# Kernel tuning notes

Measured on AMD Instinct MI355X. Metric: run time of the kernel, lower is better.

Reference implementation:

```python
import jax, jax.numpy as jnp
import numpy as np

M, IN, OUT, R = 8192, 4096, 4096, 16  # tokens, in_features, out_features, lora rank


def setup_inputs() -> dict:
    key = jax.random.key(0)
    k = jax.random.split(key, 7)
    # symmetric int8 quantized activations and weights
    x = jax.random.randint(k[0], (M, IN), -127, 128, dtype=jnp.int8)
    weight = jax.random.randint(k[1], (OUT, IN), -127, 128, dtype=jnp.int8)
    # per-token activation scales and per-output-channel weight scales
    x_scales = jax.random.uniform(k[2], (M,), jnp.float32, 0.5, 1.5) / 127.0
    scales = jax.random.uniform(k[3], (OUT,), jnp.float32, 0.5, 1.5) / 127.0
    bias = jax.random.normal(k[4], (OUT,), jnp.float32)
    # module inits lora_a ~ N(0, 1/r); lora_b is zeros in the module but we use
    # small random values so the LoRA path is numerically exercised
    lora_a = jax.random.normal(k[5], (R, IN), jnp.float32) * (1.0 / R)
    lora_b = jax.random.normal(k[6], (OUT, R), jnp.float32) * 0.02
    return dict(x=x, weight=weight, bias=bias, x_scales=x_scales,
                scales=scales, lora_a=lora_a, lora_b=lora_b, fuse_gelu=1)


def reference(x, weight, bias, x_scales, scales, lora_a, lora_b, fuse_gelu):
    acc = jax.lax.dot_general(x, weight, (((1,), (1,)), ((), ())),
                              preferred_element_type=jnp.int32)
    # dequantize with outer product of per-token and per-channel scales
    main = acc.astype(jnp.float32) * x_scales[:, None] * scales[None, :]
    # LoRA correction on the dequantized activations: (x_deq @ A^T) @ B^T
    x_deq = x.astype(jnp.float32) * x_scales[:, None]          # [M, IN]
    lora = (x_deq @ lora_a.T) @ lora_b.T                        # [M, R] @ [R, OUT]
    out = main + lora + bias[None, :]
    if fuse_gelu:  # static Python flag
        out = jax.nn.gelu(out, approximate=True)  # tanh-approx GELU (CUDA fused path)
    return out
```

## Files before the change

kernel.cpp:

```cpp
#include <hip/hip_runtime.h>

#define M_DIM 8192
#define IN_DIM 4096
#define OUT_DIM 4096

typedef int   v4i __attribute__((ext_vector_type(4)));
typedef short v8s __attribute__((ext_vector_type(8)));
typedef float v4f __attribute__((ext_vector_type(4)));

static __device__ __forceinline__ int pack4(int a, int b, int c, int d) {
    return (a & 255) | ((b & 255) << 8) | ((c & 255) << 16) | ((d & 255) << 24);
}

static __device__ __forceinline__ short f2bf(float f) {
    unsigned u = __float_as_uint(f);
    u = (u + 0x7FFFu + ((u >> 16) & 1u)) >> 16;
    return (short)u;
}

static __device__ __forceinline__ short i2bf(int v) {
    float f = (float)v;
    return (short)(__float_as_uint(f) >> 16);
}

static __device__ __forceinline__ float gelu_tanh(float u) {
    float u2 = u * u;
    float p  = fmaf(u2, 0.0356774081f, 0.7978845608f);
    float v  = u * p;
    float e  = __builtin_amdgcn_exp2f(v * 2.8853900818f);
    return u - u * __builtin_amdgcn_rcpf(e + 1.0f);
}

static __device__ __forceinline__ void async_cp16(const signed char* g, signed char* l) {
    __builtin_amdgcn_global_load_lds((const __attribute__((address_space(1))) void*)g,
                                     (__attribute__((address_space(3))) void*)l, 16, 0, 0);
}

__global__ __launch_bounds__(256) void pack_i32_i8_kernel(const int* __restrict__ src,
                                                          signed char* __restrict__ dst) {
    const int t = threadIdx.x;
    const size_t blk = (size_t)blockIdx.x;
    const int4* p = (const int4*)src + blk * 1024;
    int* q = (int*)dst + blk * 1024;
    int4 v0 = p[t], v1 = p[256 + t], v2 = p[512 + t], v3 = p[768 + t];
    q[t]       = pack4(v0.x, v0.y, v0.z, v0.w);
    q[256 + t] = pack4(v1.x, v1.y, v1.z, v1.w);
    q[512 + t] = pack4(v2.x, v2.y, v2.z, v2.w);
    q[768 + t] = pack4(v3.x, v3.y, v3.z, v3.w);
}

__global__ __launch_bounds__(256) void pack_a_kernel(const float* __restrict__ la,
                                                     short* __restrict__ a16) {
    size_t i = ((size_t)blockIdx.x * 256 + threadIdx.x) * 8;
    const float4* p = (const float4*)(la + i);
    float4 a = p[0], b = p[1];
    v8s o;
    o[0] = f2bf(a.x); o[1] = f2bf(a.y); o[2] = f2bf(a.z); o[3] = f2bf(a.w);
    o[4] = f2bf(b.x); o[5] = f2bf(b.y); o[6] = f2bf(b.z); o[7] = f2bf(b.w);
    *(v8s*)(a16 + i) = o;
}

__global__ __launch_bounds__(256) void lora_t_kernel(const signed char* __restrict__ x8,
                                                     const short* __restrict__ a16,
                                                     float* __restrict__ T) {
    __shared__ float red[4 * 256];
    const int tid = threadIdx.x;
    const int lane = tid & 63, wv = tid >> 6;
    const int fr = lane & 15, fq = lane >> 4;
    const int m0 = blockIdx.x * 16;

    const signed char* bx = x8 + (size_t)(m0 + fr) * IN_DIM + wv * 1024 + fq * 8;
    const short*       ba = a16 + (size_t)fr * IN_DIM + wv * 1024 + fq * 8;

    v4f acc = {0.f, 0.f, 0.f, 0.f};
#pragma unroll 4
    for (int kt = 0; kt < 32; ++kt) {
        int2 w = *(const int2*)(bx + kt * 32);
        int lo = w.x, hi = w.y;
        v8s xa;
        xa[0] = i2bf((lo << 24) >> 24); xa[1] = i2bf((lo << 16) >> 24);
        xa[2] = i2bf((lo << 8) >> 24);  xa[3] = i2bf(lo >> 24);
        xa[4] = i2bf((hi << 24) >> 24); xa[5] = i2bf((hi << 16) >> 24);
        xa[6] = i2bf((hi << 8) >> 24);  xa[7] = i2bf(hi >> 24);
        v8s aa = *(const v8s*)(ba + kt * 32);
        acc = __builtin_amdgcn_mfma_f32_16x16x32_bf16(xa, aa, acc, 0, 0, 0);
    }
    *(v4f*)&red[wv * 256 + lane * 4] = acc;
    __syncthreads();

    float s = red[tid] + red[256 + tid] + red[512 + tid] + red[768 + tid];
    int sl = tid >> 2, j = tid & 3;
    int row = ((sl >> 4) << 2) + j, col = sl & 15;
    T[(size_t)(m0 + row) * 16 + col] = s;
}

__global__ __launch_bounds__(256, 4) void q8_gemm_kernel(
    const signed char* __restrict__ x8, const signed char* __restrict__ w8,
    const float* __restrict__ T, const float* __restrict__ lb,
    const float* __restrict__ bias, const float* __restrict__ xsc,
    const float* __restrict__ wsc, const int* __restrict__ gflag,
    float* __restrict__ out) {
    __shared__ __align__(16) signed char smem[32768];

    const int tid  = threadIdx.x;
    const int lane = tid & 63;
    const int wv   = tid >> 6;
    const int wm   = wv >> 1;
    const int wn   = wv & 1;
    const int bn   = blockIdx.x & 31;
    const int bm   = blockIdx.x >> 5;
    const int fr   = lane & 15;
    const int fq   = lane >> 4;

    const int srow = wv * 32 + (lane >> 2);
    const int scol = (((lane & 3) ^ ((lane >> 2) & 3)) & 3) * 16;
    const signed char* ag0 = x8 + (size_t)(bm * 128 + srow) * IN_DIM + scol;
    const signed char* ag1 = ag0 + 16 * IN_DIM;
    const signed char* bg0 = w8 + (size_t)(bn * 128 + srow) * IN_DIM + scol;
    const signed char* bg1 = bg0 + 16 * IN_DIM;
    signed char* sA0 = smem + wv * 2048;
    signed char* sB0 = smem + 8192 + wv * 2048;
    signed char* sA1 = smem + 16384 + wv * 2048;
    signed char* sB1 = smem + 24576 + wv * 2048;

    v4i acc[4][4];
#pragma unroll
    for (int i = 0; i < 4; ++i)
#pragma unroll
        for (int j = 0; j < 4; ++j) acc[i][j] = 0;

    const int rot    = ((fq ^ fr) & 3) * 16;
    const int abase0 = (wm * 64 + fr) * 64 + rot;
    const int bbase0 = (wn * 64 + fr) * 64 + rot;

    async_cp16(ag0, sA0); async_cp16(ag1, sA0 + 1024);
    async_cp16(bg0, sB0); async_cp16(bg1, sB0 + 1024);

#pragma unroll 2
    for (int kk = 0; kk < 64; ++kk) {
        __syncthreads();
        if (kk + 1 < 64) {
            const size_t ko = (size_t)(kk + 1) * 64;
            if (kk & 1) {
                async_cp16(ag0 + ko, sA0); async_cp16(ag1 + ko, sA0 + 1024);
                async_cp16(bg0 + ko, sB0); async_cp16(bg1 + ko, sB0 + 1024);
            } else {
                async_cp16(ag0 + ko, sA1); async_cp16(ag1 + ko, sA1 + 1024);
                async_cp16(bg0 + ko, sB1); async_cp16(bg1 + ko, sB1 + 1024);
            }
        }
        const signed char* Ab = smem + ((kk & 1) ? 16384 : 0);
        const signed char* Bb = Ab + 8192;

        v4i av[4], bv[4];
#pragma unroll
        for (int mt = 0; mt < 4; ++mt) av[mt] = *(const v4i*)(Ab + abase0 + mt * 1024);
#pragma unroll
        for (int nt = 0; nt < 4; ++nt) bv[nt] = *(const v4i*)(Bb + bbase0 + nt * 1024);
#pragma unroll
        for (int mt = 0; mt < 4; ++mt)
#pragma unroll
            for (int nt = 0; nt < 4; ++nt)
                acc[mt][nt] = __builtin_amdgcn_mfma_i32_16x16x64_i8(av[mt], bv[nt],
                                                                    acc[mt][nt], 0, 0, 0);
    }

    __syncthreads();
    short* Tb     = (short*)smem;
    short* Bbs    = (short*)(smem + 8192);
    float* xs_t   = (float*)(smem + 16384);
    float* ws_t   = xs_t + 128;
    float* bias_t = ws_t + 128;

    {
        const int row = tid >> 1, half = tid & 1;
        const float4* tp = (const float4*)(T + (size_t)(bm * 128 + row) * 16 + half * 8);
        float4 f0 = tp[0], f1 = tp[1];
        short* dst = &Tb[row * 32 + half * 8];
        dst[0] = f2bf(f0.x); dst[1] = f2bf(f0.y); dst[2] = f2bf(f0.z); dst[3] = f2bf(f0.w);
        dst[4] = f2bf(f1.x); dst[5] = f2bf(f1.y); dst[6] = f2bf(f1.z); dst[7] = f2bf(f1.w);
        short* dz = &Tb[row * 32 + 16 + half * 8];
#pragma unroll
        for (int j = 0; j < 8; ++j) dz[j] = 0;

        const float4* bp = (const float4*)(lb + (size_t)(bn * 128 + row) * 16 + half * 8);
        float4 g0 = bp[0], g1 = bp[1];
        short* db = &Bbs[row * 32 + half * 8];
        db[0] = f2bf(g0.x); db[1] = f2bf(g0.y); db[2] = f2bf(g0.z); db[3] = f2bf(g0.w);
        db[4] = f2bf(g1.x); db[5] = f2bf(g1.y); db[6] = f2bf(g1.z); db[7] = f2bf(g1.w);
        short* dbz = &Bbs[row * 32 + 16 + half * 8];
#pragma unroll
        for (int j = 0; j < 8; ++j) dbz[j] = 0;
    }
    if (tid < 128) {
        xs_t[tid]   = xsc[bm * 128 + tid];
        ws_t[tid]   = wsc[bn * 128 + tid];
        bias_t[tid] = bias[bn * 128 + tid];
    }
    __syncthreads();

    const bool dg = (*gflag) != 0;

    v8s tb[4], bbf[4];
#pragma unroll
    for (int mt = 0; mt < 4; ++mt)
        tb[mt] = *(const v8s*)(&Tb[(wm * 64 + mt * 16 + fr) * 32 + fq * 8]);
#pragma unroll
    for (int nt = 0; nt < 4; ++nt)
        bbf[nt] = *(const v8s*)(&Bbs[(wn * 64 + nt * 16 + fr) * 32 + fq * 8]);

#pragma unroll
    for (int mt = 0; mt < 4; ++mt) {
#pragma unroll
        for (int nt = 0; nt < 4; ++nt) {
            const int ncol  = wn * 64 + nt * 16 + fr;
            const float wsv = ws_t[ncol];
            const float bv  = bias_t[ncol];
            v4f fa;
            fa[0] = (float)acc[mt][nt][0] * wsv;
            fa[1] = (float)acc[mt][nt][1] * wsv;
            fa[2] = (float)acc[mt][nt][2] * wsv;
            fa[3] = (float)acc[mt][nt][3] * wsv;
            fa = __builtin_amdgcn_mfma_f32_16x16x32_bf16(tb[mt], bbf[nt], fa, 0, 0, 0);
#pragma unroll
            for (int r = 0; r < 4; ++r) {
                const int ml = wm * 64 + mt * 16 + fq * 4 + r;
                float u = fmaf(xs_t[ml], fa[r], bv);
                if (dg) u = gelu_tanh(u);
                out[(size_t)(bm * 128 + ml) * OUT_DIM + bn * 128 + ncol] = u;
            }
        }
    }
}

extern "C" void kernel_launch(void* const* d_in, const int* in_sizes, int n_in,
                              void* d_out, int out_size, void* d_ws, size_t ws_size,
                              hipStream_t stream) {
    const int*   x     = (const int*)d_in[0];
    const int*   wt    = (const int*)d_in[1];
    const float* bias  = (const float*)d_in[2];
    const float* xsc   = (const float*)d_in[3];
    const float* wsc   = (const float*)d_in[4];
    const float* la    = (const float*)d_in[5];
    const float* lb    = (const float*)d_in[6];
    const int*   gflag = (const int*)d_in[7];
    float* out = (float*)d_out;

    signed char* x8 = (signed char*)d_ws;
    signed char* w8 = x8 + (size_t)M_DIM * IN_DIM;
    float* T = (float*)(w8 + (size_t)OUT_DIM * IN_DIM);
    short* a16 = (short*)w8;

    pack_i32_i8_kernel<<<(size_t)M_DIM * IN_DIM / 4096, 256, 0, stream>>>(x, x8);
    pack_a_kernel<<<16 * IN_DIM / (8 * 256), 256, 0, stream>>>(la, a16);
    lora_t_kernel<<<M_DIM / 16, 256, 0, stream>>>(x8, a16, T);
    pack_i32_i8_kernel<<<(size_t)OUT_DIM * IN_DIM / 4096, 256, 0, stream>>>(wt, w8);
    q8_gemm_kernel<<<(M_DIM / 128) * (OUT_DIM / 128), 256, 0, stream>>>(
        x8, w8, T, lb, bias, xsc, wsc, gflag, out);
}
```

Measured before the change: 454.5 us.

## Use 256x256 tiles with 32x32 MFMA, pre-tiled operands, fused x pack

The int8 GEMM moves from 128x128 to 256x256 block tiles using 32x32x32 i8 MFMAs. Operands are packed into an MFMA-fragment-ordered layout so each lane's LDS reads are contiguous. Packing x is fused into the LoRA T kernel, and blocks are remapped across XCDs for L2 locality. The aim is more operand reuse per byte loaded and fewer launches and passes over memory. The cost is 64KB of LDS, one block per CU, and a larger register footprint.

```diff
diff --git a/kernel.cpp b/kernel.cpp
--- a/kernel.cpp
+++ b/kernel.cpp
@@ -4,9 +4,11 @@
 #define IN_DIM 4096
 #define OUT_DIM 4096
 
-typedef int   v4i __attribute__((ext_vector_type(4)));
-typedef short v8s __attribute__((ext_vector_type(8)));
-typedef float v4f __attribute__((ext_vector_type(4)));
+typedef int   v4i  __attribute__((ext_vector_type(4)));
+typedef int   v16i __attribute__((ext_vector_type(16)));
+typedef short v8s  __attribute__((ext_vector_type(8)));
+typedef float v4f  __attribute__((ext_vector_type(4)));
+typedef float v16f __attribute__((ext_vector_type(16)));
 
 static __device__ __forceinline__ int pack4(int a, int b, int c, int d) {
     return (a & 255) | ((b & 255) << 8) | ((c & 255) << 16) | ((d & 255) << 24);
@@ -36,18 +38,6 @@
                                      (__attribute__((address_space(3))) void*)l, 16, 0, 0);
 }
 
-__global__ __launch_bounds__(256) void pack_i32_i8_kernel(const int* __restrict__ src,
-                                                          signed char* __restrict__ dst) {
-    const int t = threadIdx.x;
-    const size_t blk = (size_t)blockIdx.x;
-    const int4* p = (const int4*)src + blk * 1024;
-    int* q = (int*)dst + blk * 1024;
-    int4 v0 = p[t], v1 = p[256 + t], v2 = p[512 + t], v3 = p[768 + t];
-    q[t]       = pack4(v0.x, v0.y, v0.z, v0.w);
-    q[256 + t] = pack4(v1.x, v1.y, v1.z, v1.w);
-    q[512 + t] = pack4(v2.x, v2.y, v2.z, v2.w);
-    q[768 + t] = pack4(v3.x, v3.y, v3.z, v3.w);
-}
 
 __global__ __launch_bounds__(256) void pack_a_kernel(const float* __restrict__ la,
                                                      short* __restrict__ a16) {
@@ -60,174 +50,191 @@
     *(v8s*)(a16 + i) = o;
 }
 
-__global__ __launch_bounds__(256) void lora_t_kernel(const signed char* __restrict__ x8,
-                                                     const short* __restrict__ a16,
-                                                     float* __restrict__ T) {
+__global__ __launch_bounds__(256) void pack_w_kernel(const int* __restrict__ w,
+                                                     signed char* __restrict__ w8t) {
+    const int flat = blockIdx.x * 256 + threadIdx.x;
+    const int l  = flat & 63;
+    const int gp = (flat >> 6) & 15;
+    const int kk = (flat >> 10) & 63;
+    const int bn = flat >> 16;
+    const int n = bn * 256 + ((gp >> 1) << 5) + (l & 31);
+    const int k = kk * 64 + ((gp & 1) << 5) + ((l >> 5) << 4);
+    const int4* p = (const int4*)(w + (size_t)n * IN_DIM + k);
+    int4 a = p[0], b = p[1], c = p[2], d = p[3];
+    int4 o;
+    o.x = pack4(a.x, a.y, a.z, a.w);
+    o.y = pack4(b.x, b.y, b.z, b.w);
+    o.z = pack4(c.x, c.y, c.z, c.w);
+    o.w = pack4(d.x, d.y, d.z, d.w);
+    *(int4*)(w8t + (size_t)flat * 16) = o;
+}
+
+__global__ __launch_bounds__(256) void pack_x_lora_kernel(const int* __restrict__ x,
+                                                          const short* __restrict__ a16,
+                                                          signed char* __restrict__ x8t,
+                                                          float* __restrict__ T) {
     __shared__ float red[4 * 256];
     const int tid = threadIdx.x;
     const int lane = tid & 63, wv = tid >> 6;
     const int fr = lane & 15, fq = lane >> 4;
     const int m0 = blockIdx.x * 16;
-
-    const signed char* bx = x8 + (size_t)(m0 + fr) * IN_DIM + wv * 1024 + fq * 8;
-    const short*       ba = a16 + (size_t)fr * IN_DIM + wv * 1024 + fq * 8;
+    const int bm = m0 >> 8;
+    const int g  = (m0 >> 5) & 7;
+    const int l5 = (m0 & 16) + fr;
+    const int row = m0 + fr;
 
     v4f acc = {0.f, 0.f, 0.f, 0.f};
-#pragma unroll 4
+#pragma unroll 2
     for (int kt = 0; kt < 32; ++kt) {
-        int2 w = *(const int2*)(bx + kt * 32);
-        int lo = w.x, hi = w.y;
+        const int k  = wv * 1024 + kt * 32 + fq * 8;
+        const int4* xp = (const int4*)(x + (size_t)row * IN_DIM + k);
+        int4 a = xp[0], b = xp[1];
+        const int kk = k >> 6, c = (k >> 4) & 3, j8 = (k >> 3) & 1;
+        int2 pk = make_int2(pack4(a.x, a.y, a.z, a.w), pack4(b.x, b.y, b.z, b.w));
+        *(int2*)(x8t + ((size_t)((bm * 64 + kk) * 16 + g * 2 + (c >> 1))) * 1024 +
+                 ((c & 1) * 32 + l5) * 16 + j8 * 8) = pk;
         v8s xa;
-        xa[0] = i2bf((lo << 24) >> 24); xa[1] = i2bf((lo << 16) >> 24);
-        xa[2] = i2bf((lo << 8) >> 24);  xa[3] = i2bf(lo >> 24);
-        xa[4] = i2bf((hi << 24) >> 24); xa[5] = i2bf((hi << 16) >> 24);
-        xa[6] = i2bf((hi << 8) >> 24);  xa[7] = i2bf(hi >> 24);
-        v8s aa = *(const v8s*)(ba + kt * 32);
+        xa[0] = i2bf(a.x); xa[1] = i2bf(a.y); xa[2] = i2bf(a.z); xa[3] = i2bf(a.w);
+        xa[4] = i2bf(b.x); xa[5] = i2bf(b.y); xa[6] = i2bf(b.z); xa[7] = i2bf(b.w);
+        v8s aa = *(const v8s*)(a16 + (size_t)fr * IN_DIM + k);
         acc = __builtin_amdgcn_mfma_f32_16x16x32_bf16(xa, aa, acc, 0, 0, 0);
     }
     *(v4f*)&red[wv * 256 + lane * 4] = acc;
     __syncthreads();
 
     float s = red[tid] + red[256 + tid] + red[512 + tid] + red[768 + tid];
-    int sl = tid >> 2, j = tid & 3;
-    int row = ((sl >> 4) << 2) + j, col = sl & 15;
-    T[(size_t)(m0 + row) * 16 + col] = s;
-}
-
-__global__ __launch_bounds__(256, 4) void q8_gemm_kernel(
-    const signed char* __restrict__ x8, const signed char* __restrict__ w8,
-    const float* __restrict__ T, const float* __restrict__ lb,
+    const int sl = tid >> 2, j = tid & 3;
+    const int r16 = ((sl >> 4) << 2) + j, col = sl & 15;
+    T[(size_t)(m0 + r16) * 16 + col] = s;
+}
+
+__global__ __launch_bounds__(256, 1) void q8_gemm_kernel(
+    const signed char* __restrict__ x8t, const signed char* __restrict__ w8t,
+    const float* __restrict__ Tp, const float* __restrict__ lbm,
     const float* __restrict__ bias, const float* __restrict__ xsc,
     const float* __restrict__ wsc, const int* __restrict__ gflag,
     float* __restrict__ out) {
-    __shared__ __align__(16) signed char smem[32768];
+    __shared__ __align__(16) signed char smem[65536];
 
     const int tid  = threadIdx.x;
     const int lane = tid & 63;
     const int wv   = tid >> 6;
-    const int wm   = wv >> 1;
-    const int wn   = wv & 1;
-    const int bn   = blockIdx.x & 31;
-    const int bm   = blockIdx.x >> 5;
-    const int fr   = lane & 15;
-    const int fq   = lane >> 4;
-
-    const int srow = wv * 32 + (lane >> 2);
-    const int scol = (((lane & 3) ^ ((lane >> 2) & 3)) & 3) * 16;
-    const signed char* ag0 = x8 + (size_t)(bm * 128 + srow) * IN_DIM + scol;
-    const signed char* ag1 = ag0 + 16 * IN_DIM;
-    const signed char* bg0 = w8 + (size_t)(bn * 128 + srow) * IN_DIM + scol;
-    const signed char* bg1 = bg0 + 16 * IN_DIM;
-    signed char* sA0 = smem + wv * 2048;
-    signed char* sB0 = smem + 8192 + wv * 2048;
-    signed char* sA1 = smem + 16384 + wv * 2048;
-    signed char* sB1 = smem + 24576 + wv * 2048;
-
-    v4i acc[4][4];
-#pragma unroll
-    for (int i = 0; i < 4; ++i)
-#pragma unroll
-        for (int j = 0; j < 4; ++j) acc[i][j] = 0;
-
-    const int rot    = ((fq ^ fr) & 3) * 16;
-    const int abase0 = (wm * 64 + fr) * 64 + rot;
-    const int bbase0 = (wn * 64 + fr) * 64 + rot;
-
-    async_cp16(ag0, sA0); async_cp16(ag1, sA0 + 1024);
-    async_cp16(bg0, sB0); async_cp16(bg1, sB0 + 1024);
-
-#pragma unroll 2
+    const int wm   = wv >> 1, wn = wv & 1;
+    const int b   = blockIdx.x;
+    const int xcd = b & 7, rr = b >> 3;
+    const int bm  = xcd * 4 + (rr & 3);
+    const int bn  = rr >> 2;
+
+    const int lofs = lane * 16;
+    const signed char* Asrc = x8t + (size_t)bm * (64 * 16 * 1024);
+    const signed char* Bsrc = w8t + (size_t)bn * (64 * 16 * 1024);
+    signed char* ldsA = smem + wv * 4096;
+    signed char* ldsB = smem + 16384 + wv * 4096;
+
+    v16i acc[4][4];
+    {
+        v16i z;
+#pragma unroll
+        for (int i = 0; i < 16; ++i) z[i] = 0;
+#pragma unroll
+        for (int mt = 0; mt < 4; ++mt)
+#pragma unroll
+            for (int nt = 0; nt < 4; ++nt) acc[mt][nt] = z;
+    }
+
+    {
+        const signed char* as = Asrc + (size_t)(wv * 4) * 1024 + lofs;
+        const signed char* bs = Bsrc + (size_t)(wv * 4) * 1024 + lofs;
+#pragma unroll
+        for (int i = 0; i < 4; ++i) {
+            async_cp16(as + i * 1024, ldsA + i * 1024);
+            async_cp16(bs + i * 1024, ldsB + i * 1024);
+        }
+    }
+
     for (int kk = 0; kk < 64; ++kk) {
         __syncthreads();
         if (kk + 1 < 64) {
-            const size_t ko = (size_t)(kk + 1) * 64;
-            if (kk & 1) {
-                async_cp16(ag0 + ko, sA0); async_cp16(ag1 + ko, sA0 + 1024);
-                async_cp16(bg0 + ko, sB0); async_cp16(bg1 + ko, sB0 + 1024);
-            } else {
-                async_cp16(ag0 + ko, sA1); async_cp16(ag1 + ko, sA1 + 1024);
-                async_cp16(bg0 + ko, sB1); async_cp16(bg1 + ko, sB1 + 1024);
+            const int nb = (kk + 1) & 1;
+            const signed char* as = Asrc + ((size_t)(kk + 1) * 16 + wv * 4) * 1024 + lofs;
+            const signed char* bs = Bsrc + ((size_t)(kk + 1) * 16 + wv * 4) * 1024 + lofs;
+#pragma unroll
+            for (int i = 0; i < 4; ++i) {
+                async_cp16(as + i * 1024, ldsA + nb * 32768 + i * 1024);
+                async_cp16(bs + i * 1024, ldsB + nb * 32768 + i * 1024);
             }
         }
-        const signed char* Ab = smem + ((kk & 1) ? 16384 : 0);
-        const signed char* Bb = Ab + 8192;
-
-        v4i av[4], bv[4];
-#pragma unroll
-        for (int mt = 0; mt < 4; ++mt) av[mt] = *(const v4i*)(Ab + abase0 + mt * 1024);
-#pragma unroll
-        for (int nt = 0; nt < 4; ++nt) bv[nt] = *(const v4i*)(Bb + bbase0 + nt * 1024);
-#pragma unroll
-        for (int mt = 0; mt < 4; ++mt)
+        const signed char* Ab = smem + (kk & 1) * 32768;
+        const signed char* Bb = Ab + 16384;
+#pragma unroll
+        for (int s = 0; s < 2; ++s) {
+            v4i av[4], bv[4];
+#pragma unroll
+            for (int mt = 0; mt < 4; ++mt)
+                av[mt] = *(const v4i*)(Ab + ((wm * 4 + mt) * 2 + s) * 1024 + lofs);
 #pragma unroll
             for (int nt = 0; nt < 4; ++nt)
-                acc[mt][nt] = __builtin_amdgcn_mfma_i32_16x16x64_i8(av[mt], bv[nt],
-                                                                    acc[mt][nt], 0, 0, 0);
-    }
-
-    __syncthreads();
-    short* Tb     = (short*)smem;
-    short* Bbs    = (short*)(smem + 8192);
-    float* xs_t   = (float*)(smem + 16384);
-    float* ws_t   = xs_t + 128;
-    float* bias_t = ws_t + 128;
-
-    {
-        const int row = tid >> 1, half = tid & 1;
-        const float4* tp = (const float4*)(T + (size_t)(bm * 128 + row) * 16 + half * 8);
-        float4 f0 = tp[0], f1 = tp[1];
-        short* dst = &Tb[row * 32 + half * 8];
-        dst[0] = f2bf(f0.x); dst[1] = f2bf(f0.y); dst[2] = f2bf(f0.z); dst[3] = f2bf(f0.w);
-        dst[4] = f2bf(f1.x); dst[5] = f2bf(f1.y); dst[6] = f2bf(f1.z); dst[7] = f2bf(f1.w);
-        short* dz = &Tb[row * 32 + 16 + half * 8];
-#pragma unroll
-        for (int j = 0; j < 8; ++j) dz[j] = 0;
-
-        const float4* bp = (const float4*)(lb + (size_t)(bn * 128 + row) * 16 + half * 8);
-        float4 g0 = bp[0], g1 = bp[1];
-        short* db = &Bbs[row * 32 + half * 8];
-        db[0] = f2bf(g0.x); db[1] = f2bf(g0.y); db[2] = f2bf(g0.z); db[3] = f2bf(g0.w);
-        db[4] = f2bf(g1.x); db[5] = f2bf(g1.y); db[6] = f2bf(g1.z); db[7] = f2bf(g1.w);
-        short* dbz = &Bbs[row * 32 + 16 + half * 8];
-#pragma unroll
-        for (int j = 0; j < 8; ++j) dbz[j] = 0;
-    }
-    if (tid < 128) {
-        xs_t[tid]   = xsc[bm * 128 + tid];
-        ws_t[tid]   = wsc[bn * 128 + tid];
-        bias_t[tid] = bias[bn * 128 + tid];
-    }
-    __syncthreads();
-
+                bv[nt] = *(const v4i*)(Bb + ((wn * 4 + nt) * 2 + s) * 1024 + lofs);
+#pragma unroll
+            for (int mt = 0; mt < 4; ++mt)
+#pragma unroll
+                for (int nt = 0; nt < 4; ++nt)
+                    acc[mt][nt] = __builtin_amdgcn_mfma_i32_32x32x32_i8(
+                        av[mt], bv[nt], acc[mt][nt], 0, 0, 0);
+        }
+    }
+
+    const int mbase = bm * 256 + wm * 128;
+    const int nbase = bn * 256 + wn * 128;
+    const int l31 = lane & 31, lh = lane >> 5;
     const bool dg = (*gflag) != 0;
 
-    v8s tb[4], bbf[4];
-#pragma unroll
-    for (int mt = 0; mt < 4; ++mt)
-        tb[mt] = *(const v8s*)(&Tb[(wm * 64 + mt * 16 + fr) * 32 + fq * 8]);
-#pragma unroll
-    for (int nt = 0; nt < 4; ++nt)
-        bbf[nt] = *(const v8s*)(&Bbs[(wn * 64 + nt * 16 + fr) * 32 + fq * 8]);
-
+    v8s tf[4], bf[4];
 #pragma unroll
     for (int mt = 0; mt < 4; ++mt) {
+        const float* t0 = Tp + (size_t)(mbase + mt * 32 + l31) * 16 + lh * 8;
+        v8s v;
+#pragma unroll
+        for (int j = 0; j < 8; ++j) v[j] = f2bf(t0[j]);
+        tf[mt] = v;
+    }
+#pragma unroll
+    for (int nt = 0; nt < 4; ++nt) {
+        const float* bp = lbm + (size_t)(nbase + nt * 32 + l31) * 16 + lh * 8;
+        v8s v;
+#pragma unroll
+        for (int j = 0; j < 8; ++j) v[j] = f2bf(bp[j]);
+        bf[nt] = v;
+    }
+    float wsa[4], bba[4];
+#pragma unroll
+    for (int nt = 0; nt < 4; ++nt) {
+        const int col = nbase + nt * 32 + l31;
+        wsa[nt] = wsc[col];
+        bba[nt] = bias[col];
+    }
+
+#pragma unroll
+    for (int mt = 0; mt < 4; ++mt) {
+        const int rowb = mbase + mt * 32 + lh * 4;
+        float4 xs0 = *(const float4*)(xsc + rowb);
+        float4 xs1 = *(const float4*)(xsc + rowb + 8);
+        float4 xs2 = *(const float4*)(xsc + rowb + 16);
+        float4 xs3 = *(const float4*)(xsc + rowb + 24);
+        float xsv[16] = {xs0.x, xs0.y, xs0.z, xs0.w, xs1.x, xs1.y, xs1.z, xs1.w,
+                         xs2.x, xs2.y, xs2.z, xs2.w, xs3.x, xs3.y, xs3.z, xs3.w};
 #pragma unroll
         for (int nt = 0; nt < 4; ++nt) {
-            const int ncol  = wn * 64 + nt * 16 + fr;
-            const float wsv = ws_t[ncol];
-            const float bv  = bias_t[ncol];
-            v4f fa;
-            fa[0] = (float)acc[mt][nt][0] * wsv;
-            fa[1] = (float)acc[mt][nt][1] * wsv;
-            fa[2] = (float)acc[mt][nt][2] * wsv;
-            fa[3] = (float)acc[mt][nt][3] * wsv;
-            fa = __builtin_amdgcn_mfma_f32_16x16x32_bf16(tb[mt], bbf[nt], fa, 0, 0, 0);
-#pragma unroll
-            for (int r = 0; r < 4; ++r) {
-                const int ml = wm * 64 + mt * 16 + fq * 4 + r;
-                float u = fmaf(xs_t[ml], fa[r], bv);
+            v16f fa;
+#pragma unroll
+            for (int i = 0; i < 16; ++i) fa[i] = (float)acc[mt][nt][i] * wsa[nt];
+            fa = __builtin_amdgcn_mfma_f32_32x32x16_bf16(tf[mt], bf[nt], fa, 0, 0, 0);
+            const int col = nbase + nt * 32 + l31;
+#pragma unroll
+            for (int r = 0; r < 16; ++r) {
+                float u = fmaf(xsv[r], fa[r], bba[nt]);
                 if (dg) u = gelu_tanh(u);
-                out[(size_t)(bm * 128 + ml) * OUT_DIM + bn * 128 + ncol] = u;
+                out[(size_t)(rowb + (r & 3) + 8 * (r >> 2)) * OUT_DIM + col] = u;
             }
         }
     }
@@ -246,15 +253,14 @@
     const int*   gflag = (const int*)d_in[7];
     float* out = (float*)d_out;
 
-    signed char* x8 = (signed char*)d_ws;
-    signed char* w8 = x8 + (size_t)M_DIM * IN_DIM;
-    float* T = (float*)(w8 + (size_t)OUT_DIM * IN_DIM);
-    short* a16 = (short*)w8;
-
-    pack_i32_i8_kernel<<<(size_t)M_DIM * IN_DIM / 4096, 256, 0, stream>>>(x, x8);
+    signed char* x8t = (signed char*)d_ws;
+    signed char* w8t = x8t + (size_t)M_DIM * IN_DIM;
+    float* T = (float*)(w8t + (size_t)OUT_DIM * IN_DIM);
+    short* a16 = (short*)w8t;
+
     pack_a_kernel<<<16 * IN_DIM / (8 * 256), 256, 0, stream>>>(la, a16);
-    lora_t_kernel<<<M_DIM / 16, 256, 0, stream>>>(x8, a16, T);
-    pack_i32_i8_kernel<<<(size_t)OUT_DIM * IN_DIM / 4096, 256, 0, stream>>>(wt, w8);
-    q8_gemm_kernel<<<(M_DIM / 128) * (OUT_DIM / 128), 256, 0, stream>>>(
-        x8, w8, T, lb, bias, xsc, wsc, gflag, out);
-}
+    pack_x_lora_kernel<<<M_DIM / 16, 256, 0, stream>>>(x, a16, x8t, T);
+    pack_w_kernel<<<(size_t)OUT_DIM * IN_DIM / (16 * 256), 256, 0, stream>>>(wt, w8t);
+    q8_gemm_kernel<<<(M_DIM / 256) * (OUT_DIM / 256), 256, 0, stream>>>(
+        x8t, w8t, T, lb, bias, xsc, wsc, gflag, out);
+}
```

Result: faster. 442.9 us (-2.5%).
